# Kernel optimization log

Measured on AMD Instinct MI355X. Metric: run time of the kernel, lower is better.

## Reference

```python
import jax, jax.numpy as jnp
from jax import lax
import numpy as np

ITER_ = 10
SMOOTH = 1.0

# ---------- soft skeletonization (clDice-style, 2D) ----------

def _max_pool(x, wh, ww):
    # x: [B,1,H,W]
    return lax.reduce_window(x, -jnp.inf, lax.max, (1, 1, wh, ww), (1, 1, 1, 1), 'SAME')

def _soft_erode(x):
    return jnp.minimum(-_max_pool(-x, 3, 1), -_max_pool(-x, 1, 3))

def _soft_dilate(x):
    return _max_pool(x, 3, 3)

def _soft_open(x):
    return _soft_dilate(_soft_erode(x))

def soft_skel(img, iters):
    skel = jax.nn.relu(img - _soft_open(img))
    for _ in range(iters):
        img = _soft_erode(img)
        delta = jax.nn.relu(img - _soft_open(img))
        skel = skel + jax.nn.relu(delta - skel * delta)
    return skel

# ---------- exact 2D Euclidean distance transform ----------

def _edt2d(mask):
    # mask: [H,W] bool, True = foreground. distance to nearest background pixel.
    H, W = mask.shape
    BIG = jnp.float32(H + W)
    z = ~mask  # background indicator
    def step(d, zr):
        d = jnp.where(zr, 0.0, jnp.minimum(d + 1.0, BIG))
        return d, d
    init = jnp.full((H,), BIG, jnp.float32)
    _, f = lax.scan(step, init, z.T)            # [W,H] forward along rows
    _, b = lax.scan(step, init, z.T[::-1])      # backward
    g = jnp.minimum(f, b[::-1]).T               # [H,W] 1D row distance
    ys = jnp.arange(H, dtype=jnp.float32)
    diff2 = (ys[:, None] - ys[None, :]) ** 2    # [H,H]
    # lower envelope over columns: d2[y,x] = min_y' g[y',x]^2 + (y-y')^2
    d2 = jnp.min(g[None, :, :] ** 2 + diff2[:, :, None], axis=1)  # [H,W]
    return jnp.sqrt(d2)

_edt_batched = jax.vmap(_edt2d)  # [B,H,W] bool -> [B,H,W] float

# ---------- cbDice pieces ----------

def combine_tensors(A, B, C):
    return jnp.where((A != 0) & (B == 0), A * C, B * C)

def get_weights(mask_input, skel_input, prob_flag):
    # mask_input/skel_input: [B,H,W] float
    mask = mask_input > 0.5
    skel = skel_input > 0.5
    dist = lax.stop_gradient(_edt_batched(mask))       # EDT of binary mask, non-diff
    distances = jnp.where(mask, dist, 0.0)
    skel_radius = jnp.where(skel, distances, 0.0)
    rmax = jnp.maximum(jnp.max(skel_radius, axis=(1, 2), keepdims=True), 1.0)
    rmin = jnp.maximum(jnp.min(skel_radius, axis=(1, 2), keepdims=True), 1.0)
    d_clip = jnp.minimum(distances, rmax)
    dist_map_norm = d_clip / rmax
    skel_R_norm = skel_radius / rmax
    I_norm = (rmax - skel_radius + rmin) / rmax        # dim == 2 branch
    I_norm = jnp.where(skel, I_norm, 0.0)
    if prob_flag:
        return dist_map_norm * mask_input, skel_R_norm * mask_input, I_norm * skel_input
    m = mask.astype(jnp.float32)
    s = skel.astype(jnp.float32)
    return dist_map_norm * m, skel_R_norm * m, I_norm * s

def soft_cb_dice_loss(y_pred, y_true):
    p = jax.nn.sigmoid(y_pred)                              # [B,1,H,W]
    pb = jnp.concatenate([1.0 - p, p], axis=1)              # [B,2,H,W]
    pp = jax.nn.softmax(pb, axis=1)[:, 1]                   # [B,H,W]
    yt = jnp.where(y_true > 0, 1.0, 0.0)[:, 0]              # [B,H,W]
    hard = lax.stop_gradient((pp > 0.5).astype(jnp.float32))
    skel_pred_hard = lax.stop_gradient(soft_skel(hard[:, None], ITER_)[:, 0])
    skel_true = lax.stop_gradient(soft_skel(yt[:, None], ITER_)[:, 0])
    skel_pred_prob = skel_pred_hard * pp
    q_vl, q_slvl, q_sl = get_weights(yt, skel_true, False)
    q_vp, q_spvp, q_sp = get_weights(pp, skel_pred_prob, True)
    w_tprec = (jnp.sum(q_sp * q_vl) + SMOOTH) / (jnp.sum(combine_tensors(q_spvp, q_slvl, q_sp)) + SMOOTH)
    w_tsens = (jnp.sum(q_sl * q_vp) + SMOOTH) / (jnp.sum(combine_tensors(q_slvl, q_spvp, q_sl)) + SMOOTH)
    return 1.0 - 2.0 * (w_tprec * w_tsens) / (w_tprec + w_tsens)

def setup_inputs() -> dict:
    key = jax.random.key(0)
    k1, k2 = jax.random.split(key)
    y_pred = jax.random.normal(k1, (4, 1, 256, 256), dtype=jnp.float32)
    y_true = jax.random.randint(k2, (4, 1, 256, 256), 0, 2, dtype=jnp.int32)
    return {"y_pred": y_pred, "y_true": y_true}

def reference(y_pred, y_true):
    return soft_cb_dice_loss(y_pred, y_true)
```

## Files before the change

kernel.cpp:

```cpp
#include <hip/hip_runtime.h>

typedef unsigned long long u64;

#define NIMG 4
#define H 256
#define W 256
#define NPIX (H*W)
#define NTOT (NIMG*NPIX)
#define WPR 4
#define WPI (H*WPR)
#define WPB (NIMG*WPI)
#define XT 16
#define NSKEL 8
#define NEDT 128
#define NB2 (NSKEL+NEDT)
#define NB3 (NTOT/1024)

__device__ __forceinline__ void erode_from(const u64 S[][WPR], int y, u64 out[WPR]) {
  u64 c[WPR], up[WPR], dn[WPR];
#pragma unroll
  for (int k = 0; k < WPR; ++k) {
    c[k]  = S[y][k];
    up[k] = (y > 0)     ? S[y-1][k] : ~0ULL;
    dn[k] = (y < H-1)   ? S[y+1][k] : ~0ULL;
  }
#pragma unroll
  for (int k = 0; k < WPR; ++k) {
    u64 l = (c[k] << 1) | ((k > 0)     ? (c[k-1] >> 63) : 1ULL);
    u64 r = (c[k] >> 1) | ((k < WPR-1) ? (c[k+1] << 63) : 0x8000000000000000ULL);
    out[k] = c[k] & up[k] & dn[k] & l & r;
  }
}

__device__ __forceinline__ void dilate_from(const u64 S[][WPR], int y, u64 out[WPR]) {
  u64 v[WPR];
#pragma unroll
  for (int k = 0; k < WPR; ++k) {
    u64 a = S[y][k];
    if (y > 0)   a |= S[y-1][k];
    if (y < H-1) a |= S[y+1][k];
    v[k] = a;
  }
#pragma unroll
  for (int k = 0; k < WPR; ++k) {
    u64 l = (v[k] << 1) | ((k > 0)     ? (v[k-1] >> 63) : 0ULL);
    u64 r = (v[k] >> 1) | ((k < WPR-1) ? (v[k+1] << 63) : 0ULL);
    out[k] = v[k] | l | r;
  }
}

__global__ void __launch_bounds__(256) prep_kernel(
    const float* __restrict__ y_pred, const int* __restrict__ y_true,
    float* __restrict__ pp, u64* __restrict__ mask_bits,
    unsigned* __restrict__ rmm_u, double* __restrict__ sums,
    unsigned* __restrict__ cnts) {
  if (blockIdx.x == 0) {
    if (threadIdx.x < 16) rmm_u[threadIdx.x] = (threadIdx.x & 1) ? 0x7F800000u : 0u;
    else if (threadIdx.x < 20) sums[threadIdx.x - 16] = 0.0;
    else if (threadIdx.x < 29) cnts[threadIdx.x - 20] = 0u;
  }
  int i = blockIdx.x * 256 + threadIdx.x;
  float x = y_pred[i];
  float p = 1.0f / (1.0f + expf(-x));
  float q = 1.0f / (1.0f + expf(-(2.0f * p - 1.0f)));
  pp[i] = q;
  u64 bt = __ballot(y_true[i] > 0);
  u64 bp = __ballot(q > 0.5f);
  if ((threadIdx.x & 63) == 0) {
    mask_bits[i >> 6] = bt;
    mask_bits[WPB + (i >> 6)] = bp;
  }
}

__global__ void __launch_bounds__(256, 1) morpho_kernel(
    const u64* __restrict__ mask_bits, u64* __restrict__ skel_bits,
    float* __restrict__ edt, unsigned* __restrict__ rmm_u,
    unsigned* __restrict__ cnts) {
  __shared__ u64 SA[H][WPR];
  __shared__ u64 SB[H][WPR];
  __shared__ float col2[H][XT + 1];
  __shared__ u64 srow[H];
  __shared__ float smax[4], smin[4];
  int t = threadIdx.x;

  if (blockIdx.x < NSKEL) {
    int bi = blockIdx.x;
    int y = t;
    int base = bi * WPI;
    u64 a[WPR], cur[WPR], e[WPR], d[WPR], sk[WPR];
#pragma unroll
    for (int k = 0; k < WPR; ++k) { a[k] = mask_bits[base + y*WPR + k]; SA[y][k] = a[k]; }
    __syncthreads();
    erode_from(SA, y, e);
#pragma unroll
    for (int k = 0; k < WPR; ++k) SB[y][k] = e[k];
    __syncthreads();
    dilate_from(SB, y, d);
#pragma unroll
    for (int k = 0; k < WPR; ++k) { sk[k] = a[k] & ~d[k]; cur[k] = e[k]; }
    u64 (*P)[WPR] = SB;
    u64 (*Q)[WPR] = SA;
    for (int it = 0; it < 10; ++it) {
      erode_from(P, y, e);
#pragma unroll
      for (int k = 0; k < WPR; ++k) Q[y][k] = e[k];
      __syncthreads();
      dilate_from(Q, y, d);
#pragma unroll
      for (int k = 0; k < WPR; ++k) { sk[k] |= cur[k] & ~d[k]; cur[k] = e[k]; }
      u64 (*T)[WPR] = P; P = Q; Q = T;
    }
#pragma unroll
    for (int k = 0; k < WPR; ++k) skel_bits[base + y*WPR + k] = sk[k];
    __syncthreads();
    if (t == 0) {
      __threadfence();
      atomicAdd(&cnts[bi], 1u);
    }
  } else {
    int bt = blockIdx.x - NSKEL;
    int bi = bt >> 4;
    int xt = bt & 15;
    int x0 = xt * XT;
    int kx = x0 >> 6;
    int sh0 = x0 & 63;
    {
      int y = t;
      const u64* row = mask_bits + bi*WPI + y*WPR;
      u64 z[WPR];
#pragma unroll
      for (int k = 0; k < WPR; ++k) z[k] = ~row[k];
#pragma unroll
      for (int xx = 0; xx < XT; ++xx) {
        int x = x0 + xx;
        int bx = x & 63;
        int ld = 512;
        {
          u64 w = z[kx] & ((bx == 63) ? ~0ULL : ((1ULL << (bx+1)) - 1ULL));
          for (int k = kx; ; ) {
            if (w) { int pos = 63 - __builtin_clzll(w) + (k << 6); ld = x - pos; break; }
            if (--k < 0) break;
            w = z[k];
          }
        }
        int rd = 512;
        {
          u64 w = z[kx] & (~0ULL << bx);
          for (int k = kx; ; ) {
            if (w) { int pos = __builtin_ctzll(w) + (k << 6); rd = pos - x; break; }
            if (++k > WPR-1) break;
            w = z[k];
          }
        }
        int g = min(ld, rd);
        col2[y][xx] = (float)(g * g);
      }
    }
    __syncthreads();
    int x  = t & (XT - 1);
    int yg = t >> 4;
    float dist_r[16];
#pragma unroll
    for (int j = 0; j < 16; ++j) {
      int y = yg * 16 + j;
      float best = col2[y][x];
      for (int k = 1; k < H; ++k) {
        float k2 = (float)(k * k);
        if (k2 >= best) break;
        int ym = y - k, yq = y + k;
        if (ym >= 0) best = fminf(best, col2[ym][x] + k2);
        if (yq < H)  best = fminf(best, col2[yq][x] + k2);
      }
      float dist = sqrtf(best);
      dist_r[j] = dist;
      edt[bi*NPIX + y*W + x0 + x] = dist;
    }
    if (t == 0) {
      while (__hip_atomic_load(&cnts[bi], __ATOMIC_RELAXED,
                               __HIP_MEMORY_SCOPE_AGENT) == 0u)
        __builtin_amdgcn_s_sleep(2);
    }
    __syncthreads();
    srow[t] = __hip_atomic_load(&skel_bits[bi*WPI + t*WPR + kx],
                                __ATOMIC_RELAXED, __HIP_MEMORY_SCOPE_AGENT);
    __syncthreads();
    float vmax = 0.0f, vmin = 3.0e38f;
#pragma unroll
    for (int j = 0; j < 16; ++j) {
      int y = yg * 16 + j;
      u64 sw = srow[y];
      int sb = (int)((sw >> (sh0 + x)) & 1ULL);
      float srad = sb ? dist_r[j] : 0.0f;
      vmax = fmaxf(vmax, srad);
      vmin = fminf(vmin, srad);
    }
    for (int o = 32; o > 0; o >>= 1) {
      vmax = fmaxf(vmax, __shfl_down(vmax, o, 64));
      vmin = fminf(vmin, __shfl_down(vmin, o, 64));
    }
    int wave = t >> 6, lane = t & 63;
    if (lane == 0) { smax[wave] = vmax; smin[wave] = vmin; }
    __syncthreads();
    if (t == 0) {
      float mx = smax[0], mn = smin[0];
      for (int wv = 1; wv < 4; ++wv) { mx = fmaxf(mx, smax[wv]); mn = fminf(mn, smin[wv]); }
      atomicMax(&rmm_u[bi*2 + 0], __float_as_uint(mx));
      atomicMin(&rmm_u[bi*2 + 1], __float_as_uint(mn));
    }
  }
}

__global__ void __launch_bounds__(256) final_kernel(
    const float* __restrict__ edt, const u64* __restrict__ mask_bits,
    const u64* __restrict__ skel_bits, const float* __restrict__ pp,
    const unsigned* __restrict__ rmm_u, double* __restrict__ sums,
    unsigned* __restrict__ cnts, float* __restrict__ out) {
  int i0 = (blockIdx.x * 256 + threadIdx.x) * 4;
  int img = i0 >> 16;
  int wi = i0 >> 6;
  int b0 = i0 & 63;
  u64 mw_t = mask_bits[wi];
  u64 sw_t = skel_bits[wi];
  u64 sw_p = skel_bits[WPB + wi];
  float4 d_t4 = *(const float4*)(edt + i0);
  float4 d_p4 = *(const float4*)(edt + NTOT + i0);
  float4 pp4  = *(const float4*)(pp + i0);
  float rmax_t = fmaxf(__uint_as_float(rmm_u[img*2 + 0]), 1.0f);
  float rmin_t = fmaxf(__uint_as_float(rmm_u[img*2 + 1]), 1.0f);
  float rmax_p = fmaxf(__uint_as_float(rmm_u[(4+img)*2 + 0]), 1.0f);
  float rmin_p = fmaxf(__uint_as_float(rmm_u[(4+img)*2 + 1]), 1.0f);
  float t1 = 0.f, t2 = 0.f, t3 = 0.f, t4 = 0.f;
  float dts[4] = {d_t4.x, d_t4.y, d_t4.z, d_t4.w};
  float dps[4] = {d_p4.x, d_p4.y, d_p4.z, d_p4.w};
  float pps[4] = {pp4.x, pp4.y, pp4.z, pp4.w};
#pragma unroll
  for (int j = 0; j < 4; ++j) {
    int b = b0 + j;
    int m_t = (int)((mw_t >> b) & 1ULL);
    int s_t = (int)((sw_t >> b) & 1ULL);
    float distances_t = m_t ? dts[j] : 0.0f;
    float skelrad_t   = s_t ? distances_t : 0.0f;
    float dmn_t = fminf(distances_t, rmax_t) / rmax_t;
    float srn_t = skelrad_t / rmax_t;
    float In_t  = s_t ? (rmax_t - skelrad_t + rmin_t) / rmax_t : 0.0f;
    float q_vl   = m_t ? dmn_t : 0.0f;
    float q_slvl = m_t ? srn_t : 0.0f;
    float q_sl   = s_t ? In_t  : 0.0f;
    int s_pb = (int)((sw_p >> b) & 1ULL);
    float ppv = pps[j];
    float skel_in_p = s_pb ? ppv : 0.0f;
    bool msk_p = ppv > 0.5f;
    bool sk_p  = skel_in_p > 0.5f;
    float distances_p = msk_p ? dps[j] : 0.0f;
    float skelrad_p   = sk_p ? distances_p : 0.0f;
    float dmn_p = fminf(distances_p, rmax_p) / rmax_p;
    float srn_p = skelrad_p / rmax_p;
    float In_p  = sk_p ? (rmax_p - skelrad_p + rmin_p) / rmax_p : 0.0f;
    float q_vp   = dmn_p * ppv;
    float q_spvp = srn_p * ppv;
    float q_sp   = In_p * skel_in_p;
    t1 += q_sp * q_vl;
    t2 += (q_spvp != 0.0f && q_slvl == 0.0f) ? q_spvp * q_sp : q_slvl * q_sp;
    t3 += q_sl * q_vp;
    t4 += (q_slvl != 0.0f && q_spvp == 0.0f) ? q_slvl * q_sl : q_spvp * q_sl;
  }
  for (int o = 32; o > 0; o >>= 1) {
    t1 += __shfl_down(t1, o, 64);
    t2 += __shfl_down(t2, o, 64);
    t3 += __shfl_down(t3, o, 64);
    t4 += __shfl_down(t4, o, 64);
  }
  __shared__ float part[4][4];
  int wave = threadIdx.x >> 6, lane = threadIdx.x & 63;
  if (lane == 0) { part[wave][0]=t1; part[wave][1]=t2; part[wave][2]=t3; part[wave][3]=t4; }
  __syncthreads();
  if (threadIdx.x == 0) {
    float a0=0,a1=0,a2=0,a3=0;
    for (int wv = 0; wv < 4; ++wv) {
      a0 += part[wv][0]; a1 += part[wv][1]; a2 += part[wv][2]; a3 += part[wv][3];
    }
    atomicAdd(&sums[0], (double)a0);
    atomicAdd(&sums[1], (double)a1);
    atomicAdd(&sums[2], (double)a2);
    atomicAdd(&sums[3], (double)a3);
    __threadfence();
    unsigned c = atomicAdd(&cnts[8], 1u);
    if (c == NB3 - 1) {
      double s0 = atomicAdd(&sums[0], 0.0);
      double s1 = atomicAdd(&sums[1], 0.0);
      double s2 = atomicAdd(&sums[2], 0.0);
      double s3 = atomicAdd(&sums[3], 0.0);
      double wp  = (s0 + 1.0) / (s1 + 1.0);
      double wsn = (s2 + 1.0) / (s3 + 1.0);
      out[0] = (float)(1.0 - 2.0 * (wp * wsn) / (wp + wsn));
    }
  }
}

extern "C" void kernel_launch(void* const* d_in, const int* in_sizes, int n_in,
                              void* d_out, int out_size, void* d_ws, size_t ws_size,
                              hipStream_t stream) {
  (void)in_sizes; (void)n_in; (void)out_size; (void)ws_size;
  const float* y_pred = (const float*)d_in[0];
  const int*   y_true = (const int*)d_in[1];
  float* out = (float*)d_out;
  char* ws = (char*)d_ws;

  float* pp        = (float*)(ws + 0);
  float* edt       = (float*)(ws + 1048576);
  u64*   mask_bits = (u64*)  (ws + 3145728);
  u64*   skel_bits = (u64*)  (ws + 3211264);
  unsigned* rmm_u  = (unsigned*)(ws + 3276800);
  double* sums     = (double*)(ws + 3276864);
  unsigned* cnts   = (unsigned*)(ws + 3276896);

  prep_kernel<<<NTOT/256, 256, 0, stream>>>(y_pred, y_true, pp, mask_bits, rmm_u, sums, cnts);
  morpho_kernel<<<NB2, 256, 0, stream>>>(mask_bits, skel_bits, edt, rmm_u, cnts);
  final_kernel<<<NB3, 256, 0, stream>>>(edt, mask_bits, skel_bits, pp, rmm_u, sums, cnts, out);
}
```

Measured before the change: 90.03 us.

## Fuse final reduction into morpho kernel with grid-wide spin barrier

Merges the final reduction kernel into the morphology/EDT kernel. The EDT blocks wait on a global counter until all skeleton and EDT blocks finish, then each handles 8 pixels of the loss reduction. The prep kernel no longer writes the pp array; the sigmoid is recomputed from y_pred in the fused stage. This removes one launch and a pp round-trip through memory, but relies on all 136 blocks being co-resident and leaves 8 skeleton blocks idle during the reduction stage.

```diff
diff --git a/kernel.cpp b/kernel.cpp
--- a/kernel.cpp
+++ b/kernel.cpp
@@ -14,7 +14,6 @@
 #define NSKEL 8
 #define NEDT 128
 #define NB2 (NSKEL+NEDT)
-#define NB3 (NTOT/1024)
 
 __device__ __forceinline__ void erode_from(const u64 S[][WPR], int y, u64 out[WPR]) {
   u64 c[WPR], up[WPR], dn[WPR];
@@ -51,19 +50,17 @@
 
 __global__ void __launch_bounds__(256) prep_kernel(
     const float* __restrict__ y_pred, const int* __restrict__ y_true,
-    float* __restrict__ pp, u64* __restrict__ mask_bits,
-    unsigned* __restrict__ rmm_u, double* __restrict__ sums,
-    unsigned* __restrict__ cnts) {
+    u64* __restrict__ mask_bits, unsigned* __restrict__ rmm_u,
+    double* __restrict__ sums, unsigned* __restrict__ cnts) {
   if (blockIdx.x == 0) {
     if (threadIdx.x < 16) rmm_u[threadIdx.x] = (threadIdx.x & 1) ? 0x7F800000u : 0u;
     else if (threadIdx.x < 20) sums[threadIdx.x - 16] = 0.0;
-    else if (threadIdx.x < 29) cnts[threadIdx.x - 20] = 0u;
+    else if (threadIdx.x < 30) cnts[threadIdx.x - 20] = 0u;
   }
   int i = blockIdx.x * 256 + threadIdx.x;
   float x = y_pred[i];
   float p = 1.0f / (1.0f + expf(-x));
   float q = 1.0f / (1.0f + expf(-(2.0f * p - 1.0f)));
-  pp[i] = q;
   u64 bt = __ballot(y_true[i] > 0);
   u64 bp = __ballot(q > 0.5f);
   if ((threadIdx.x & 63) == 0) {
@@ -72,15 +69,18 @@
   }
 }
 
-__global__ void __launch_bounds__(256, 1) morpho_kernel(
+__global__ void __launch_bounds__(256, 1) morpho_final_kernel(
+    const float* __restrict__ y_pred, const int* __restrict__ y_true,
     const u64* __restrict__ mask_bits, u64* __restrict__ skel_bits,
     float* __restrict__ edt, unsigned* __restrict__ rmm_u,
-    unsigned* __restrict__ cnts) {
+    double* __restrict__ sums, unsigned* __restrict__ cnts,
+    float* __restrict__ out) {
   __shared__ u64 SA[H][WPR];
   __shared__ u64 SB[H][WPR];
   __shared__ float col2[H][XT + 1];
   __shared__ u64 srow[H];
   __shared__ float smax[4], smin[4];
+  __shared__ float part[4][4];
   int t = threadIdx.x;
 
   if (blockIdx.x < NSKEL) {
@@ -116,8 +116,12 @@
     if (t == 0) {
       __threadfence();
       atomicAdd(&cnts[bi], 1u);
-    }
-  } else {
+      atomicAdd(&cnts[9], 1u);
+    }
+    return;
+  }
+
+  {
     int bt = blockIdx.x - NSKEL;
     int bi = bt >> 4;
     int xt = bt & 15;
@@ -206,93 +210,100 @@
       for (int wv = 1; wv < 4; ++wv) { mx = fmaxf(mx, smax[wv]); mn = fminf(mn, smin[wv]); }
       atomicMax(&rmm_u[bi*2 + 0], __float_as_uint(mx));
       atomicMin(&rmm_u[bi*2 + 1], __float_as_uint(mn));
-    }
-  }
-}
-
-__global__ void __launch_bounds__(256) final_kernel(
-    const float* __restrict__ edt, const u64* __restrict__ mask_bits,
-    const u64* __restrict__ skel_bits, const float* __restrict__ pp,
-    const unsigned* __restrict__ rmm_u, double* __restrict__ sums,
-    unsigned* __restrict__ cnts, float* __restrict__ out) {
-  int i0 = (blockIdx.x * 256 + threadIdx.x) * 4;
-  int img = i0 >> 16;
-  int wi = i0 >> 6;
-  int b0 = i0 & 63;
-  u64 mw_t = mask_bits[wi];
-  u64 sw_t = skel_bits[wi];
-  u64 sw_p = skel_bits[WPB + wi];
-  float4 d_t4 = *(const float4*)(edt + i0);
-  float4 d_p4 = *(const float4*)(edt + NTOT + i0);
-  float4 pp4  = *(const float4*)(pp + i0);
-  float rmax_t = fmaxf(__uint_as_float(rmm_u[img*2 + 0]), 1.0f);
-  float rmin_t = fmaxf(__uint_as_float(rmm_u[img*2 + 1]), 1.0f);
-  float rmax_p = fmaxf(__uint_as_float(rmm_u[(4+img)*2 + 0]), 1.0f);
-  float rmin_p = fmaxf(__uint_as_float(rmm_u[(4+img)*2 + 1]), 1.0f);
-  float t1 = 0.f, t2 = 0.f, t3 = 0.f, t4 = 0.f;
-  float dts[4] = {d_t4.x, d_t4.y, d_t4.z, d_t4.w};
-  float dps[4] = {d_p4.x, d_p4.y, d_p4.z, d_p4.w};
-  float pps[4] = {pp4.x, pp4.y, pp4.z, pp4.w};
-#pragma unroll
-  for (int j = 0; j < 4; ++j) {
-    int b = b0 + j;
-    int m_t = (int)((mw_t >> b) & 1ULL);
-    int s_t = (int)((sw_t >> b) & 1ULL);
-    float distances_t = m_t ? dts[j] : 0.0f;
-    float skelrad_t   = s_t ? distances_t : 0.0f;
-    float dmn_t = fminf(distances_t, rmax_t) / rmax_t;
-    float srn_t = skelrad_t / rmax_t;
-    float In_t  = s_t ? (rmax_t - skelrad_t + rmin_t) / rmax_t : 0.0f;
-    float q_vl   = m_t ? dmn_t : 0.0f;
-    float q_slvl = m_t ? srn_t : 0.0f;
-    float q_sl   = s_t ? In_t  : 0.0f;
-    int s_pb = (int)((sw_p >> b) & 1ULL);
-    float ppv = pps[j];
-    float skel_in_p = s_pb ? ppv : 0.0f;
-    bool msk_p = ppv > 0.5f;
-    bool sk_p  = skel_in_p > 0.5f;
-    float distances_p = msk_p ? dps[j] : 0.0f;
-    float skelrad_p   = sk_p ? distances_p : 0.0f;
-    float dmn_p = fminf(distances_p, rmax_p) / rmax_p;
-    float srn_p = skelrad_p / rmax_p;
-    float In_p  = sk_p ? (rmax_p - skelrad_p + rmin_p) / rmax_p : 0.0f;
-    float q_vp   = dmn_p * ppv;
-    float q_spvp = srn_p * ppv;
-    float q_sp   = In_p * skel_in_p;
-    t1 += q_sp * q_vl;
-    t2 += (q_spvp != 0.0f && q_slvl == 0.0f) ? q_spvp * q_sp : q_slvl * q_sp;
-    t3 += q_sl * q_vp;
-    t4 += (q_slvl != 0.0f && q_spvp == 0.0f) ? q_slvl * q_sl : q_spvp * q_sl;
-  }
-  for (int o = 32; o > 0; o >>= 1) {
-    t1 += __shfl_down(t1, o, 64);
-    t2 += __shfl_down(t2, o, 64);
-    t3 += __shfl_down(t3, o, 64);
-    t4 += __shfl_down(t4, o, 64);
-  }
-  __shared__ float part[4][4];
-  int wave = threadIdx.x >> 6, lane = threadIdx.x & 63;
-  if (lane == 0) { part[wave][0]=t1; part[wave][1]=t2; part[wave][2]=t3; part[wave][3]=t4; }
-  __syncthreads();
-  if (threadIdx.x == 0) {
-    float a0=0,a1=0,a2=0,a3=0;
-    for (int wv = 0; wv < 4; ++wv) {
-      a0 += part[wv][0]; a1 += part[wv][1]; a2 += part[wv][2]; a3 += part[wv][3];
-    }
-    atomicAdd(&sums[0], (double)a0);
-    atomicAdd(&sums[1], (double)a1);
-    atomicAdd(&sums[2], (double)a2);
-    atomicAdd(&sums[3], (double)a3);
+      __threadfence();
+      atomicAdd(&cnts[9], 1u);
+      while (__hip_atomic_load(&cnts[9], __ATOMIC_RELAXED,
+                               __HIP_MEMORY_SCOPE_AGENT) < NB2)
+        __builtin_amdgcn_s_sleep(2);
+    }
+    __syncthreads();
     __threadfence();
-    unsigned c = atomicAdd(&cnts[8], 1u);
-    if (c == NB3 - 1) {
-      double s0 = atomicAdd(&sums[0], 0.0);
-      double s1 = atomicAdd(&sums[1], 0.0);
-      double s2 = atomicAdd(&sums[2], 0.0);
-      double s3 = atomicAdd(&sums[3], 0.0);
-      double wp  = (s0 + 1.0) / (s1 + 1.0);
-      double wsn = (s2 + 1.0) / (s3 + 1.0);
-      out[0] = (float)(1.0 - 2.0 * (wp * wsn) / (wp + wsn));
+  }
+
+  {
+    int fb = blockIdx.x - NSKEL;
+    int i0 = (fb * 256 + t) * 8;
+    int img = i0 >> 16;
+    int wi  = i0 >> 6;
+    int b0  = i0 & 63;
+    u64 mw_t = mask_bits[wi];
+    u64 sw_t = skel_bits[wi];
+    u64 sw_p = skel_bits[WPB + wi];
+    float4 xp0 = *(const float4*)(y_pred + i0);
+    float4 xp1 = *(const float4*)(y_pred + i0 + 4);
+    float4 dt0 = *(const float4*)(edt + i0);
+    float4 dt1 = *(const float4*)(edt + i0 + 4);
+    float4 dp0 = *(const float4*)(edt + NTOT + i0);
+    float4 dp1 = *(const float4*)(edt + NTOT + i0 + 4);
+    float rmax_t = fmaxf(__uint_as_float(rmm_u[img*2 + 0]), 1.0f);
+    float rmin_t = fmaxf(__uint_as_float(rmm_u[img*2 + 1]), 1.0f);
+    float rmax_p = fmaxf(__uint_as_float(rmm_u[(4+img)*2 + 0]), 1.0f);
+    float rmin_p = fmaxf(__uint_as_float(rmm_u[(4+img)*2 + 1]), 1.0f);
+    float xs[8] = {xp0.x,xp0.y,xp0.z,xp0.w,xp1.x,xp1.y,xp1.z,xp1.w};
+    float dts[8] = {dt0.x,dt0.y,dt0.z,dt0.w,dt1.x,dt1.y,dt1.z,dt1.w};
+    float dps[8] = {dp0.x,dp0.y,dp0.z,dp0.w,dp1.x,dp1.y,dp1.z,dp1.w};
+    float q1 = 0.f, q2 = 0.f, q3 = 0.f, q4 = 0.f;
+#pragma unroll
+    for (int j = 0; j < 8; ++j) {
+      int b = b0 + j;
+      float p = 1.0f / (1.0f + expf(-xs[j]));
+      float ppv = 1.0f / (1.0f + expf(-(2.0f * p - 1.0f)));
+      int m_t = (int)((mw_t >> b) & 1ULL);
+      int s_t = (int)((sw_t >> b) & 1ULL);
+      float distances_t = m_t ? dts[j] : 0.0f;
+      float skelrad_t   = s_t ? distances_t : 0.0f;
+      float dmn_t = fminf(distances_t, rmax_t) / rmax_t;
+      float srn_t = skelrad_t / rmax_t;
+      float In_t  = s_t ? (rmax_t - skelrad_t + rmin_t) / rmax_t : 0.0f;
+      float q_vl   = m_t ? dmn_t : 0.0f;
+      float q_slvl = m_t ? srn_t : 0.0f;
+      float q_sl   = s_t ? In_t  : 0.0f;
+      int s_pb = (int)((sw_p >> b) & 1ULL);
+      float skel_in_p = s_pb ? ppv : 0.0f;
+      bool msk_p = ppv > 0.5f;
+      bool sk_p  = skel_in_p > 0.5f;
+      float distances_p = msk_p ? dps[j] : 0.0f;
+      float skelrad_p   = sk_p ? distances_p : 0.0f;
+      float dmn_p = fminf(distances_p, rmax_p) / rmax_p;
+      float srn_p = skelrad_p / rmax_p;
+      float In_p  = sk_p ? (rmax_p - skelrad_p + rmin_p) / rmax_p : 0.0f;
+      float q_vp   = dmn_p * ppv;
+      float q_spvp = srn_p * ppv;
+      float q_sp   = In_p * skel_in_p;
+      q1 += q_sp * q_vl;
+      q2 += (q_spvp != 0.0f && q_slvl == 0.0f) ? q_spvp * q_sp : q_slvl * q_sp;
+      q3 += q_sl * q_vp;
+      q4 += (q_slvl != 0.0f && q_spvp == 0.0f) ? q_slvl * q_sl : q_spvp * q_sl;
+    }
+    for (int o = 32; o > 0; o >>= 1) {
+      q1 += __shfl_down(q1, o, 64);
+      q2 += __shfl_down(q2, o, 64);
+      q3 += __shfl_down(q3, o, 64);
+      q4 += __shfl_down(q4, o, 64);
+    }
+    int wave = t >> 6, lane = t & 63;
+    if (lane == 0) { part[wave][0]=q1; part[wave][1]=q2; part[wave][2]=q3; part[wave][3]=q4; }
+    __syncthreads();
+    if (t == 0) {
+      float a0=0,a1=0,a2=0,a3=0;
+      for (int wv = 0; wv < 4; ++wv) {
+        a0 += part[wv][0]; a1 += part[wv][1]; a2 += part[wv][2]; a3 += part[wv][3];
+      }
+      atomicAdd(&sums[0], (double)a0);
+      atomicAdd(&sums[1], (double)a1);
+      atomicAdd(&sums[2], (double)a2);
+      atomicAdd(&sums[3], (double)a3);
+      __threadfence();
+      unsigned c = atomicAdd(&cnts[8], 1u);
+      if (c == NEDT - 1) {
+        double s0 = atomicAdd(&sums[0], 0.0);
+        double s1 = atomicAdd(&sums[1], 0.0);
+        double s2 = atomicAdd(&sums[2], 0.0);
+        double s3 = atomicAdd(&sums[3], 0.0);
+        double wp  = (s0 + 1.0) / (s1 + 1.0);
+        double wsn = (s2 + 1.0) / (s3 + 1.0);
+        out[0] = (float)(1.0 - 2.0 * (wp * wsn) / (wp + wsn));
+      }
     }
   }
 }
@@ -306,15 +317,14 @@
   float* out = (float*)d_out;
   char* ws = (char*)d_ws;
 
-  float* pp        = (float*)(ws + 0);
-  float* edt       = (float*)(ws + 1048576);
-  u64*   mask_bits = (u64*)  (ws + 3145728);
-  u64*   skel_bits = (u64*)  (ws + 3211264);
-  unsigned* rmm_u  = (unsigned*)(ws + 3276800);
-  double* sums     = (double*)(ws + 3276864);
-  unsigned* cnts   = (unsigned*)(ws + 3276896);
-
-  prep_kernel<<<NTOT/256, 256, 0, stream>>>(y_pred, y_true, pp, mask_bits, rmm_u, sums, cnts);
-  morpho_kernel<<<NB2, 256, 0, stream>>>(mask_bits, skel_bits, edt, rmm_u, cnts);
-  final_kernel<<<NB3, 256, 0, stream>>>(edt, mask_bits, skel_bits, pp, rmm_u, sums, cnts, out);
-}
+  float* edt       = (float*)(ws + 0);
+  u64*   mask_bits = (u64*)  (ws + 2097152);
+  u64*   skel_bits = (u64*)  (ws + 2162688);
+  unsigned* rmm_u  = (unsigned*)(ws + 2228224);
+  double* sums     = (double*)(ws + 2228288);
+  unsigned* cnts   = (unsigned*)(ws + 2228320);
+
+  prep_kernel<<<NTOT/256, 256, 0, stream>>>(y_pred, y_true, mask_bits, rmm_u, sums, cnts);
+  morpho_final_kernel<<<NB2, 256, 0, stream>>>(y_pred, y_true, mask_bits, skel_bits,
+                                               edt, rmm_u, sums, cnts, out);
+}
```

New measurement: 94.40 us. 4.9% more time.
